# Optimization experiments

Measured on AMD Instinct MI355X. Metric: run time of the kernel, lower is better.

The kernel has to match this reference:

```python
import jax, jax.numpy as jnp
import numpy as np

N, H, C, G = 50000, 16, 8, 128   # nodes, heads, per-head channels, graphs
F_IN, NUM_CLASSES = 128, 2
E = 800000
HC = H * C
NEG_SLOPE = 0.2
BN_EPS = 1e-5


def setup_inputs() -> dict:
    key = jax.random.key(0)
    ks = jax.random.split(key, 32)
    s = 0.1
    p = lambda k, shape: (jax.random.normal(k, shape, jnp.float32) * s)
    inp = {
        "x": jax.random.normal(ks[0], (N, F_IN), jnp.float32),
        "edge_index": jax.random.randint(ks[1], (2, E), 0, N, dtype=jnp.int32),
        "batch": jnp.sort(jax.random.randint(ks[2], (N,), 0, G, dtype=jnp.int32)),
        # GAT layer 1 (in=F_IN)
        "W1": p(ks[3], (F_IN, HC)), "b1": p(ks[4], (HC,)),
        "asrc1": p(ks[5], (H, C)), "adst1": p(ks[6], (H, C)),
        "g1": 1.0 + p(ks[7], (HC,)), "beta1": p(ks[8], (HC,)),
        # GAT layer 2 (in=HC)
        "W2": p(ks[9], (HC, HC)), "b2": p(ks[10], (HC,)),
        "asrc2": p(ks[11], (H, C)), "adst2": p(ks[12], (H, C)),
        "g2": 1.0 + p(ks[13], (HC,)), "beta2": p(ks[14], (HC,)),
        # GAT layer 3
        "W3": p(ks[15], (HC, HC)), "b3": p(ks[16], (HC,)),
        "asrc3": p(ks[17], (H, C)), "adst3": p(ks[18], (H, C)),
        "g3": 1.0 + p(ks[19], (HC,)), "beta3": p(ks[20], (HC,)),
        # final linear + bn4
        "Wl": p(ks[21], (2 * HC, NUM_CLASSES)), "bl": p(ks[22], (NUM_CLASSES,)),
        "g4": 1.0 + p(ks[23], (NUM_CLASSES,)), "beta4": p(ks[24], (NUM_CLASSES,)),
    }
    return inp


def _gat(x, src, dst, W, b, asrc, adst):
    # x: [N, F_in] -> h: [N, H, C]
    h = (x @ W).reshape(N, H, C)
    a_s = jnp.einsum("nhc,hc->nh", h, asrc)  # [N,H]
    a_d = jnp.einsum("nhc,hc->nh", h, adst)
    e = jax.nn.leaky_relu(a_s[src] + a_d[dst], NEG_SLOPE)  # [E',H]
    # per-destination softmax (every node has a self loop -> segments non-empty)
    e_max = jax.ops.segment_max(e, dst, num_segments=N)
    ex = jnp.exp(e - e_max[dst])
    denom = jax.ops.segment_sum(ex, dst, num_segments=N)
    alpha = ex / (denom[dst] + 1e-16)  # [E',H]
    out = jax.ops.segment_sum(h[src] * alpha[:, :, None], dst, num_segments=N)
    return out.reshape(N, HC) + b


def _bn(x, g, beta):
    mu = jnp.mean(x, axis=0)
    var = jnp.mean((x - mu) ** 2, axis=0)  # biased, training-mode BN
    return (x - mu) * jax.lax.rsqrt(var + BN_EPS) * g + beta


def reference(x, edge_index, batch,
              W1, b1, asrc1, adst1, g1, beta1,
              W2, b2, asrc2, adst2, g2, beta2,
              W3, b3, asrc3, adst3, g3, beta3,
              Wl, bl, g4, beta4):
    # add self loops once (add_self_loops=True in every GATConv)
    loop = jnp.arange(N, dtype=edge_index.dtype)
    src = jnp.concatenate([edge_index[0], loop])
    dst = jnp.concatenate([edge_index[1], loop])

    h = jax.nn.relu(_bn(_gat(x, src, dst, W1, b1, asrc1, adst1), g1, beta1))
    h = jax.nn.relu(_bn(_gat(h, src, dst, W2, b2, asrc2, adst2), g2, beta2))
    h = jax.nn.relu(_bn(_gat(h, src, dst, W3, b3, asrc3, adst3), g3, beta3))

    pooled_sum = jax.ops.segment_sum(h, batch, num_segments=G)        # [G,HC]
    cnt = jax.ops.segment_sum(jnp.ones((N,), h.dtype), batch, num_segments=G)
    pooled_mean = pooled_sum / jnp.maximum(cnt, 1.0)[:, None]
    z = jnp.concatenate([pooled_mean, pooled_sum], axis=1)            # [G,2*HC]
    z = z @ Wl + bl
    return _bn(z, g4, beta4)
```

## Files before the change

kernel.cpp:

```cpp
#include <hip/hip_runtime.h>

#define NN 50000
#define NHEADS 16
#define NGRAPH 128
#define NEDGE 800000
#define NEP (NEDGE + NN)

#define EPB 2048
#define NBLK 416
#define NBUK 391

typedef float4 f4;
typedef __attribute__((ext_vector_type(4))) float f32x4;
typedef __attribute__((ext_vector_type(8))) short s8;

__device__ inline unsigned short f2b(float f) {
  union { float f; unsigned u; } v; v.f = f;
  unsigned r = v.u + 0x7FFFu + ((v.u >> 16) & 1u);
  return (unsigned short)(r >> 16);
}
__device__ inline float b2f(unsigned u16) {
  union { unsigned u; float f; } v; v.u = u16 << 16;
  return v.f;
}


__global__ __launch_bounds__(256) void k_hist(const int* __restrict__ ei, int* __restrict__ counts) {
  int i = blockIdx.x * 256 + threadIdx.x;
  if (i >= NEP) return;
  int d = (i < NEDGE) ? ei[NEDGE + i] : (i - NEDGE);
  atomicAdd(&counts[d], 1);
}

__global__ __launch_bounds__(256) void k_scan1(const int* __restrict__ counts, int* __restrict__ row_off, int* __restrict__ blk_tot) {
  __shared__ int buf[256];
  int t = threadIdx.x;
  int i = blockIdx.x * 256 + t;
  int v = (i < NN) ? counts[i] : 0;
  buf[t] = v;
  __syncthreads();
  for (int off = 1; off < 256; off <<= 1) {
    int y = (t >= off) ? buf[t - off] : 0;
    __syncthreads();
    buf[t] += y;
    __syncthreads();
  }
  if (i < NN) row_off[i] = buf[t] - v;
  if (t == 255) blk_tot[blockIdx.x] = buf[255];
}

__global__ __launch_bounds__(256) void k_scan2(const int* __restrict__ blk_tot, int* __restrict__ blk_off, int* __restrict__ row_off, int nb) {
  __shared__ int buf[256];
  int t = threadIdx.x;
  int v = (t < nb) ? blk_tot[t] : 0;
  buf[t] = v;
  __syncthreads();
  for (int off = 1; off < 256; off <<= 1) {
    int y = (t >= off) ? buf[t - off] : 0;
    __syncthreads();
    buf[t] += y;
    __syncthreads();
  }
  if (t < nb) blk_off[t] = buf[t] - v;
  if (t == 255) row_off[NN] = buf[255];
}

__global__ __launch_bounds__(256) void k_scan3(int* __restrict__ row_off, const int* __restrict__ blk_off) {
  int i = blockIdx.x * 256 + threadIdx.x;
  if (i < NN) row_off[i] += blk_off[blockIdx.x];
}


__global__ __launch_bounds__(256) void k_bhist(const int* __restrict__ ei, int* __restrict__ cntmat) {
  __shared__ int hist[NBUK];
  int t = threadIdx.x, b = blockIdx.x;
  for (int k = t; k < NBUK; k += 256) hist[k] = 0;
  __syncthreads();
  int i0 = b * EPB;
  int i1 = i0 + EPB < NEP ? i0 + EPB : NEP;
  for (int i = i0 + t; i < i1; i += 256) {
    int d = (i < NEDGE) ? ei[NEDGE + i] : (i - NEDGE);
    atomicAdd(&hist[d >> 7], 1);
  }
  __syncthreads();
  for (int k = t; k < NBUK; k += 256) cntmat[b * NBUK + k] = hist[k];
}

__global__ __launch_bounds__(512) void k_bscan(int* __restrict__ cntmat) {
  __shared__ int buf[512];
  int t = threadIdx.x, k = blockIdx.x;
  int v = (t < NBLK) ? cntmat[t * NBUK + k] : 0;
  buf[t] = v;
  __syncthreads();
  for (int off = 1; off < 512; off <<= 1) {
    int y = (t >= off) ? buf[t - off] : 0;
    __syncthreads();
    buf[t] += y;
    __syncthreads();
  }
  if (t < NBLK) cntmat[t * NBUK + k] = buf[t] - v;
}

__global__ __launch_bounds__(256) void k_bscatter(const int* __restrict__ ei, const int* __restrict__ cntmat,
                                                  const int* __restrict__ row_off, unsigned* __restrict__ pairs) {
  __shared__ int cur[NBUK];
  int t = threadIdx.x, b = blockIdx.x;
  for (int k = t; k < NBUK; k += 256) cur[k] = row_off[k << 7] + cntmat[b * NBUK + k];
  __syncthreads();
  int i0 = b * EPB;
  int i1 = i0 + EPB < NEP ? i0 + EPB : NEP;
  for (int i = i0 + t; i < i1; i += 256) {
    int s, d;
    if (i < NEDGE) { s = ei[i]; d = ei[NEDGE + i]; }
    else { s = d = i - NEDGE; }
    int pos = atomicAdd(&cur[d >> 7], 1);
    pairs[pos] = ((unsigned)(d & 127) << 16) | (unsigned)s;
  }
}

__global__ __launch_bounds__(256) void k_bfinal(const unsigned* __restrict__ pairs,
                                                const int* __restrict__ row_off, int* __restrict__ colp) {
  __shared__ int cur[128];
  int t = threadIdx.x, k = blockIdx.x;
  int n0 = k << 7;
  if (t < 128 && n0 + t < NN) cur[t] = row_off[n0 + t];
  __syncthreads();
  int nend = (k + 1) << 7; if (nend > NN) nend = NN;
  int p0 = row_off[n0], p1 = row_off[nend];
  for (int i = p0 + t; i < p1; i += 256) {
    unsigned r = pairs[i];
    int pos = atomicAdd(&cur[r >> 16], 1);
    colp[pos] = (int)(r & 0xffffu);
  }
}


__global__ __launch_bounds__(256) void k_cast(const float* __restrict__ X, unsigned short* __restrict__ Xb, int total8) {
  int i = blockIdx.x * 256 + threadIdx.x;
  if (i >= total8) return;
  const f4* X4 = (const f4*)X;
  f4 a = X4[2 * i], b = X4[2 * i + 1];
  uint4 o;
  o.x = (unsigned)f2b(a.x) | ((unsigned)f2b(a.y) << 16);
  o.y = (unsigned)f2b(a.z) | ((unsigned)f2b(a.w) << 16);
  o.z = (unsigned)f2b(b.x) | ((unsigned)f2b(b.y) << 16);
  o.w = (unsigned)f2b(b.z) | ((unsigned)f2b(b.w) << 16);
  ((uint4*)Xb)[i] = o;
}


__global__ __launch_bounds__(256) void k_wt(const float* __restrict__ W0, const float* __restrict__ W1, const float* __restrict__ W2,
                                            unsigned short* __restrict__ T0, unsigned short* __restrict__ T1, unsigned short* __restrict__ T2) {
  int idx = blockIdx.x * 256 + threadIdx.x;
  int L = idx >> 14, r = idx & 16383;
  int n = r >> 7, k = r & 127;
  const float* W = (L == 0) ? W0 : (L == 1) ? W1 : W2;
  unsigned short* T = (L == 0) ? T0 : (L == 1) ? T1 : T2;
  T[n * 128 + k] = f2b(W[k * 128 + n]);
}


__global__ __launch_bounds__(256) void k_gemm(const unsigned short* __restrict__ Xb, const unsigned short* __restrict__ Wt,
                                              unsigned short* __restrict__ Hb) {
  int w = threadIdx.x >> 6, l = threadIdx.x & 63;
  int r0 = blockIdx.x * 128 + w * 32;
  int lr = l & 15, lg = l >> 4;
  f32x4 acc[2][8];
#pragma unroll
  for (int m = 0; m < 2; ++m)
#pragma unroll
    for (int n = 0; n < 8; ++n) acc[m][n] = (f32x4){0.f, 0.f, 0.f, 0.f};

#pragma unroll
  for (int ks = 0; ks < 4; ++ks) {
    int koff = ks * 32 + lg * 8;
    s8 a[2];
#pragma unroll
    for (int m = 0; m < 2; ++m) {
      int row = r0 + m * 16 + lr;
      row = (row < NN) ? row : (NN - 1);
      a[m] = *(const s8*)(Xb + (size_t)row * 128 + koff);
    }
    s8 b[8];
#pragma unroll
    for (int n = 0; n < 8; ++n)
      b[n] = *(const s8*)(Wt + (size_t)(n * 16 + lr) * 128 + koff);
#pragma unroll
    for (int m = 0; m < 2; ++m)
#pragma unroll
      for (int n = 0; n < 8; ++n)
        acc[m][n] = __builtin_amdgcn_mfma_f32_16x16x32_bf16(a[m], b[n], acc[m][n], 0, 0, 0);
  }

#pragma unroll
  for (int m = 0; m < 2; ++m) {
    int rowb = r0 + m * 16 + lg * 4;
#pragma unroll
    for (int n = 0; n < 8; ++n) {
      int colb = n * 16 + lr;
#pragma unroll
      for (int reg = 0; reg < 4; ++reg) {
        int row = rowb + reg;
        if (row < NN) Hb[(size_t)row * 128 + colb] = f2b(acc[m][n][reg]);
      }
    }
  }
}


__global__ __launch_bounds__(256) void k_coef(const unsigned short* __restrict__ Hb, const float* __restrict__ asrc,
                                              const float* __restrict__ adst, unsigned short* __restrict__ Asb, float* __restrict__ Ad) {
  int idx = blockIdx.x * 256 + threadIdx.x;
  if (idx >= NN * NHEADS) return;
  int n = idx >> 4, hd = idx & 15;
  uint4 hv = *(const uint4*)(Hb + (size_t)n * 128 + hd * 8);
  float h0 = b2f(hv.x & 0xffff), h1 = b2f(hv.x >> 16);
  float h2 = b2f(hv.y & 0xffff), h3 = b2f(hv.y >> 16);
  float h4 = b2f(hv.z & 0xffff), h5 = b2f(hv.z >> 16);
  float h6 = b2f(hv.w & 0xffff), h7 = b2f(hv.w >> 16);
  const f4* s4 = (const f4*)(asrc + hd * 8);
  const f4* d4 = (const f4*)(adst + hd * 8);
  f4 sa = s4[0], sb = s4[1], da = d4[0], db = d4[1];
  float as_v = h0 * sa.x + h1 * sa.y + h2 * sa.z + h3 * sa.w + h4 * sb.x + h5 * sb.y + h6 * sb.z + h7 * sb.w;
  float ad_v = h0 * da.x + h1 * da.y + h2 * da.z + h3 * da.w + h4 * db.x + h5 * db.y + h6 * db.z + h7 * db.w;
  Asb[idx] = f2b(as_v);
  Ad[idx] = ad_v;
}


__global__ __launch_bounds__(256) void k_agg(const unsigned short* __restrict__ Hb, const unsigned short* __restrict__ Asb,
                                             const float* __restrict__ Ad,
                                             const int* __restrict__ row_off, const int* __restrict__ col,
                                             unsigned short* __restrict__ Vb) {
  int node = blockIdx.x * 8 + (threadIdx.x >> 5);
  int l = threadIdx.x & 31;
  int h = l & 15, par = l >> 4;
  int e0 = row_off[node], e1 = row_off[node + 1];
  float adh = Ad[node * 16 + h];
  float den = 0.f;
  float acc[8] = {0.f, 0.f, 0.f, 0.f, 0.f, 0.f, 0.f, 0.f};
  int j = e0 + par;
  for (; j + 6 < e1; j += 8) {
    int s0 = col[j], s1 = col[j + 2], s2 = col[j + 4], s3 = col[j + 6];
    float a0 = b2f(Asb[s0 * 16 + h]), a1 = b2f(Asb[s1 * 16 + h]);
    float a2 = b2f(Asb[s2 * 16 + h]), a3 = b2f(Asb[s3 * 16 + h]);
    uint4 p0 = *(const uint4*)(Hb + (size_t)s0 * 128 + h * 8);
    uint4 p1 = *(const uint4*)(Hb + (size_t)s1 * 128 + h * 8);
    uint4 p2 = *(const uint4*)(Hb + (size_t)s2 * 128 + h * 8);
    uint4 p3 = *(const uint4*)(Hb + (size_t)s3 * 128 + h * 8);
    a0 += adh; a1 += adh; a2 += adh; a3 += adh;
    a0 = (a0 > 0.f) ? a0 : 0.2f * a0;  a1 = (a1 > 0.f) ? a1 : 0.2f * a1;
    a2 = (a2 > 0.f) ? a2 : 0.2f * a2;  a3 = (a3 > 0.f) ? a3 : 0.2f * a3;
    float x0 = __expf(a0), x1 = __expf(a1), x2 = __expf(a2), x3 = __expf(a3);
    den += (x0 + x1) + (x2 + x3);
    acc[0] += x0 * b2f(p0.x & 0xffff) + x1 * b2f(p1.x & 0xffff) + x2 * b2f(p2.x & 0xffff) + x3 * b2f(p3.x & 0xffff);
    acc[1] += x0 * b2f(p0.x >> 16)    + x1 * b2f(p1.x >> 16)    + x2 * b2f(p2.x >> 16)    + x3 * b2f(p3.x >> 16);
    acc[2] += x0 * b2f(p0.y & 0xffff) + x1 * b2f(p1.y & 0xffff) + x2 * b2f(p2.y & 0xffff) + x3 * b2f(p3.y & 0xffff);
    acc[3] += x0 * b2f(p0.y >> 16)    + x1 * b2f(p1.y >> 16)    + x2 * b2f(p2.y >> 16)    + x3 * b2f(p3.y >> 16);
    acc[4] += x0 * b2f(p0.z & 0xffff) + x1 * b2f(p1.z & 0xffff) + x2 * b2f(p2.z & 0xffff) + x3 * b2f(p3.z & 0xffff);
    acc[5] += x0 * b2f(p0.z >> 16)    + x1 * b2f(p1.z >> 16)    + x2 * b2f(p2.z >> 16)    + x3 * b2f(p3.z >> 16);
    acc[6] += x0 * b2f(p0.w & 0xffff) + x1 * b2f(p1.w & 0xffff) + x2 * b2f(p2.w & 0xffff) + x3 * b2f(p3.w & 0xffff);
    acc[7] += x0 * b2f(p0.w >> 16)    + x1 * b2f(p1.w >> 16)    + x2 * b2f(p2.w >> 16)    + x3 * b2f(p3.w >> 16);
  }
  for (; j < e1; j += 2) {
    int s0 = col[j];
    float a0 = b2f(Asb[s0 * 16 + h]) + adh;
    uint4 p0 = *(const uint4*)(Hb + (size_t)s0 * 128 + h * 8);
    a0 = (a0 > 0.f) ? a0 : 0.2f * a0;
    float x0 = __expf(a0);
    den += x0;
    acc[0] += x0 * b2f(p0.x & 0xffff);
    acc[1] += x0 * b2f(p0.x >> 16);
    acc[2] += x0 * b2f(p0.y & 0xffff);
    acc[3] += x0 * b2f(p0.y >> 16);
    acc[4] += x0 * b2f(p0.z & 0xffff);
    acc[5] += x0 * b2f(p0.z >> 16);
    acc[6] += x0 * b2f(p0.w & 0xffff);
    acc[7] += x0 * b2f(p0.w >> 16);
  }
  den += __shfl_xor(den, 16);
#pragma unroll
  for (int k = 0; k < 8; ++k) acc[k] += __shfl_xor(acc[k], 16);
  if (par == 0) {
    float inv = 1.f / (den + 1e-16f);
    uint4 o;
    o.x = (unsigned)f2b(acc[0] * inv) | ((unsigned)f2b(acc[1] * inv) << 16);
    o.y = (unsigned)f2b(acc[2] * inv) | ((unsigned)f2b(acc[3] * inv) << 16);
    o.z = (unsigned)f2b(acc[4] * inv) | ((unsigned)f2b(acc[5] * inv) << 16);
    o.w = (unsigned)f2b(acc[6] * inv) | ((unsigned)f2b(acc[7] * inv) << 16);
    *(uint4*)(Vb + (size_t)node * 128 + h * 8) = o;
  }
}


#define BN_CHUNK 391

__global__ __launch_bounds__(256) void k_bnreduce(const unsigned short* __restrict__ Vb, float* __restrict__ partS, float* __restrict__ partQ) {
  int t = threadIdx.x;
  int c4 = t & 31, rs = t >> 5;
  int r0 = blockIdx.x * BN_CHUNK + rs;
  int rend = blockIdx.x * BN_CHUNK + BN_CHUNK;
  if (rend > NN) rend = NN;
  float s0 = 0.f, s1 = 0.f, s2 = 0.f, s3 = 0.f;
  float q0 = 0.f, q1 = 0.f, q2 = 0.f, q3 = 0.f;
  for (int r = r0; r < rend; r += 8) {
    uint2 p = *(const uint2*)(Vb + (size_t)r * 128 + c4 * 4);
    float v0 = b2f(p.x & 0xffff), v1 = b2f(p.x >> 16);
    float v2 = b2f(p.y & 0xffff), v3 = b2f(p.y >> 16);
    s0 += v0; s1 += v1; s2 += v2; s3 += v3;
    q0 += v0 * v0; q1 += v1 * v1; q2 += v2 * v2; q3 += v3 * v3;
  }
  __shared__ float sm[8][32][8];
  sm[rs][c4][0] = s0; sm[rs][c4][1] = s1; sm[rs][c4][2] = s2; sm[rs][c4][3] = s3;
  sm[rs][c4][4] = q0; sm[rs][c4][5] = q1; sm[rs][c4][6] = q2; sm[rs][c4][7] = q3;
  __syncthreads();
  if (t < 32) {
#pragma unroll
    for (int k = 0; k < 4; ++k) {
      float S = 0.f, Q = 0.f;
#pragma unroll
      for (int r = 0; r < 8; ++r) { S += sm[r][t][k]; Q += sm[r][t][4 + k]; }
      partS[blockIdx.x * 128 + t * 4 + k] = S;
      partQ[blockIdx.x * 128 + t * 4 + k] = Q;
    }
  }
}

__global__ __launch_bounds__(512) void k_bnfin(const float* __restrict__ partS, const float* __restrict__ partQ,
                                               const float* __restrict__ gam, const float* __restrict__ bet,
                                               float* __restrict__ sc) {
  int t = threadIdx.x;
  int c = t & 127, q = (t >> 7) & 1, hf = t >> 8;
  const float* src = q ? partQ : partS;
  float s = 0.f;
#pragma unroll 8
  for (int i = hf * 64; i < hf * 64 + 64; ++i) s += src[i * 128 + c];
  __shared__ float sm[512];
  sm[t] = s;
  __syncthreads();
  if (t < 128) {
    float S = sm[t] + sm[t + 256];
    float Q = sm[t + 128] + sm[t + 384];
    float mean = S * (1.f / NN);
    float var = fmaxf(Q * (1.f / NN) - mean * mean, 0.f);
    float sg = gam[t] * rsqrtf(var + 1e-5f);
    sc[t] = sg;
    sc[128 + t] = bet[t] - mean * sg;
  }
}

__global__ __launch_bounds__(256) void k_bnapply(const unsigned short* __restrict__ Vb, unsigned short* __restrict__ Xb,
                                                 const float* __restrict__ sc) {
  int idx = blockIdx.x * 256 + threadIdx.x;
  int c4 = idx & 31;
  uint2 p = ((const uint2*)Vb)[idx];
  f4 s = ((const f4*)sc)[c4], sh = ((const f4*)sc)[32 + c4];
  float v0 = fmaxf(b2f(p.x & 0xffff) * s.x + sh.x, 0.f);
  float v1 = fmaxf(b2f(p.x >> 16)    * s.y + sh.y, 0.f);
  float v2 = fmaxf(b2f(p.y & 0xffff) * s.z + sh.z, 0.f);
  float v3 = fmaxf(b2f(p.y >> 16)    * s.w + sh.w, 0.f);
  uint2 o;
  o.x = (unsigned)f2b(v0) | ((unsigned)f2b(v1) << 16);
  o.y = (unsigned)f2b(v2) | ((unsigned)f2b(v3) << 16);
  ((uint2*)Xb)[idx] = o;
}


__global__ __launch_bounds__(256) void k_gb(const int* __restrict__ batch, int* __restrict__ gstart) {
  int g = threadIdx.x;
  if (g > NGRAPH) return;
  int lo = 0, hi = NN;
  while (lo < hi) { int mid = (lo + hi) >> 1; if (batch[mid] < g) lo = mid + 1; else hi = mid; }
  gstart[g] = lo;
}

__global__ __launch_bounds__(256) void k_pool(const unsigned short* __restrict__ Vb, const int* __restrict__ gstart,
                                              float* __restrict__ pooled) {
  int g = blockIdx.x >> 2, chunk = blockIdx.x & 3;
  int t = threadIdx.x;
  int c4 = t & 31, rs = t >> 5;
  int r0 = gstart[g], r1 = gstart[g + 1];
  float s0 = 0.f, s1 = 0.f, s2 = 0.f, s3 = 0.f;
  for (int r = r0 + chunk + 4 * rs + (c4 & 0) ; r < r1; r += 32) {
    uint2 p = *(const uint2*)(Vb + (size_t)r * 128 + c4 * 4);
    s0 += b2f(p.x & 0xffff); s1 += b2f(p.x >> 16);
    s2 += b2f(p.y & 0xffff); s3 += b2f(p.y >> 16);
  }
  __shared__ float sm[8][32][4];
  sm[rs][c4][0] = s0; sm[rs][c4][1] = s1; sm[rs][c4][2] = s2; sm[rs][c4][3] = s3;
  __syncthreads();
  if (t < 32) {
#pragma unroll
    for (int k = 0; k < 4; ++k) {
      float S = 0.f;
#pragma unroll
      for (int r = 0; r < 8; ++r) S += sm[r][t][k];
      atomicAdd(&pooled[g * 128 + t * 4 + k], S);
    }
  }
}

__global__ __launch_bounds__(256) void k_final(const float* __restrict__ pooled, const int* __restrict__ gstart,
                                               const float* __restrict__ Wl, const float* __restrict__ bl,
                                               const float* __restrict__ g4, const float* __restrict__ b4,
                                               float* __restrict__ out) {
  int t = threadIdx.x;
  int g = t >> 1, cls = t & 1;
  float cnt = fmaxf((float)(gstart[g + 1] - gstart[g]), 1.f);
  float inv = 1.f / cnt;
  float z = bl[cls];
  for (int f = 0; f < 128; ++f) {
    float ps = pooled[g * 128 + f];
    z += ps * inv * Wl[f * 2 + cls] + ps * Wl[(128 + f) * 2 + cls];
  }
  __shared__ float zs[256];
  __shared__ float st[4];
  zs[t] = z;
  __syncthreads();
  if (t < 2) {
    float s = 0.f, s2 = 0.f;
    for (int gg = 0; gg < 128; ++gg) { float v = zs[gg * 2 + t]; s += v; s2 += v * v; }
    float mean = s * (1.f / 128.f);
    float var = s2 * (1.f / 128.f) - mean * mean;
    var = fmaxf(var, 0.f);
    float sc = g4[t] * rsqrtf(var + 1e-5f);
    st[t] = sc; st[2 + t] = b4[t] - mean * sc;
  }
  __syncthreads();
  out[t] = zs[t] * st[cls] + st[2 + cls];
}


extern "C" void kernel_launch(void* const* d_in, const int* in_sizes, int n_in,
                              void* d_out, int out_size, void* d_ws, size_t ws_size,
                              hipStream_t stream) {
  const float* x     = (const float*)d_in[0];
  const int*   ei    = (const int*)d_in[1];
  const int*   batch = (const int*)d_in[2];
  const float* W[3]    = {(const float*)d_in[3],  (const float*)d_in[9],  (const float*)d_in[15]};
  const float* asrc[3] = {(const float*)d_in[5],  (const float*)d_in[11], (const float*)d_in[17]};
  const float* adst[3] = {(const float*)d_in[6],  (const float*)d_in[12], (const float*)d_in[18]};
  const float* gam[3]  = {(const float*)d_in[7],  (const float*)d_in[13], (const float*)d_in[19]};
  const float* bet[3]  = {(const float*)d_in[8],  (const float*)d_in[14], (const float*)d_in[20]};
  const float* Wl    = (const float*)d_in[21];
  const float* bl    = (const float*)d_in[22];
  const float* g4    = (const float*)d_in[23];
  const float* beta4 = (const float*)d_in[24];

  char* ws = (char*)d_ws;
  size_t off = 0;
  auto alloc = [&](size_t bytes) -> void* {
    void* p = (void*)(ws + off);
    off += (bytes + 255) & ~(size_t)255;
    return p;
  };

  int* counts   = (int*)alloc((size_t)NN * 4);
  int* row_off  = (int*)alloc((size_t)(NN + 1) * 4);
  int* col      = (int*)alloc((size_t)NEP * 4);
  int* blk_tot  = (int*)alloc(256 * 4);
  int* blk_off  = (int*)alloc(256 * 4);
  int* cntmat   = (int*)alloc((size_t)NBLK * NBUK * 4);
  unsigned* pairs = (unsigned*)alloc((size_t)NEP * 4);
  unsigned short* Xb = (unsigned short*)alloc((size_t)NN * 128 * 2);
  unsigned short* Hb = (unsigned short*)alloc((size_t)NN * 128 * 2);
  unsigned short* Vb = (unsigned short*)alloc((size_t)NN * 128 * 2);
  unsigned short* Asb = (unsigned short*)alloc((size_t)NN * 16 * 2);
  float* Ad     = (float*)alloc((size_t)NN * 16 * 4);
  unsigned short* Wt0 = (unsigned short*)alloc(16384 * 2);
  unsigned short* Wt1 = (unsigned short*)alloc(16384 * 2);
  unsigned short* Wt2 = (unsigned short*)alloc(16384 * 2);
  const unsigned short* Wt[3] = {Wt0, Wt1, Wt2};
  float* partS  = (float*)alloc(128 * 128 * 4);
  float* partQ  = (float*)alloc(128 * 128 * 4);
  float* bn_sc  = (float*)alloc(256 * 4);
  float* pooled = (float*)alloc((size_t)NGRAPH * 128 * 4);
  int* gstart   = (int*)alloc((size_t)(NGRAPH + 1) * 4);

  hipMemsetAsync(counts, 0, (size_t)NN * 4, stream);
  k_hist<<<(NEP + 255) / 256, 256, 0, stream>>>(ei, counts);
  k_scan1<<<(NN + 255) / 256, 256, 0, stream>>>(counts, row_off, blk_tot);
  k_scan2<<<1, 256, 0, stream>>>(blk_tot, blk_off, row_off, (NN + 255) / 256);
  k_scan3<<<(NN + 255) / 256, 256, 0, stream>>>(row_off, blk_off);

  k_bhist<<<NBLK, 256, 0, stream>>>(ei, cntmat);
  k_bscan<<<NBUK, 512, 0, stream>>>(cntmat);
  k_bscatter<<<NBLK, 256, 0, stream>>>(ei, cntmat, row_off, pairs);
  k_bfinal<<<NBUK, 256, 0, stream>>>(pairs, row_off, col);

  k_wt<<<192, 256, 0, stream>>>(W[0], W[1], W[2], Wt0, Wt1, Wt2);
  k_cast<<<(NN * 16 + 255) / 256, 256, 0, stream>>>(x, Xb, NN * 16);
  k_gb<<<1, 256, 0, stream>>>(batch, gstart);

  hipMemsetAsync(pooled, 0, (size_t)NGRAPH * 128 * 4, stream);

  for (int L = 0; L < 3; ++L) {
    k_gemm<<<(NN + 127) / 128, 256, 0, stream>>>(Xb, Wt[L], Hb);
    k_coef<<<(NN * 16) / 256, 256, 0, stream>>>(Hb, asrc[L], adst[L], Asb, Ad);
    k_agg<<<NN / 8, 256, 0, stream>>>(Hb, Asb, Ad, row_off, col, Vb);
    k_bnreduce<<<128, 256, 0, stream>>>(Vb, partS, partQ);
    k_bnfin<<<1, 512, 0, stream>>>(partS, partQ, gam[L], bet[L], bn_sc);
    k_bnapply<<<(NN * 32) / 256, 256, 0, stream>>>(Vb, Xb, bn_sc);
  }

  k_pool<<<NGRAPH * 4, 256, 0, stream>>>(Xb, gstart, pooled);
  k_final<<<1, 256, 0, stream>>>(pooled, gstart, Wl, bl, g4, beta4, (float*)d_out);
}
```

Baseline: 349.4 us.

## Build CSR from bucket sort alone, merge prep kernels, unroll aggregation deeper

Removes the separate per-node histogram and three-pass scan. Bucket totals are now scanned in k_bbase, and k_bfinal derives per-node row offsets by counting and scanning inside each 128-node bucket. The cast, weight-transpose and graph-boundary kernels are merged into one launch to cut launch overhead. The aggregation edge loop is also unrolled to 8 edges per iteration, giving more loads in flight at the cost of extra registers.

```diff
diff --git a/kernel.cpp b/kernel.cpp
--- a/kernel.cpp
+++ b/kernel.cpp
@@ -9,6 +9,8 @@
 #define EPB 2048
 #define NBLK 416
 #define NBUK 391
+#define CASTB 3125
+#define WTB 192
 
 typedef float4 f4;
 typedef __attribute__((ext_vector_type(4))) float f32x4;
@@ -22,52 +24,6 @@
 __device__ inline float b2f(unsigned u16) {
   union { unsigned u; float f; } v; v.u = u16 << 16;
   return v.f;
-}
-
-
-__global__ __launch_bounds__(256) void k_hist(const int* __restrict__ ei, int* __restrict__ counts) {
-  int i = blockIdx.x * 256 + threadIdx.x;
-  if (i >= NEP) return;
-  int d = (i < NEDGE) ? ei[NEDGE + i] : (i - NEDGE);
-  atomicAdd(&counts[d], 1);
-}
-
-__global__ __launch_bounds__(256) void k_scan1(const int* __restrict__ counts, int* __restrict__ row_off, int* __restrict__ blk_tot) {
-  __shared__ int buf[256];
-  int t = threadIdx.x;
-  int i = blockIdx.x * 256 + t;
-  int v = (i < NN) ? counts[i] : 0;
-  buf[t] = v;
-  __syncthreads();
-  for (int off = 1; off < 256; off <<= 1) {
-    int y = (t >= off) ? buf[t - off] : 0;
-    __syncthreads();
-    buf[t] += y;
-    __syncthreads();
-  }
-  if (i < NN) row_off[i] = buf[t] - v;
-  if (t == 255) blk_tot[blockIdx.x] = buf[255];
-}
-
-__global__ __launch_bounds__(256) void k_scan2(const int* __restrict__ blk_tot, int* __restrict__ blk_off, int* __restrict__ row_off, int nb) {
-  __shared__ int buf[256];
-  int t = threadIdx.x;
-  int v = (t < nb) ? blk_tot[t] : 0;
-  buf[t] = v;
-  __syncthreads();
-  for (int off = 1; off < 256; off <<= 1) {
-    int y = (t >= off) ? buf[t - off] : 0;
-    __syncthreads();
-    buf[t] += y;
-    __syncthreads();
-  }
-  if (t < nb) blk_off[t] = buf[t] - v;
-  if (t == 255) row_off[NN] = buf[255];
-}
-
-__global__ __launch_bounds__(256) void k_scan3(int* __restrict__ row_off, const int* __restrict__ blk_off) {
-  int i = blockIdx.x * 256 + threadIdx.x;
-  if (i < NN) row_off[i] += blk_off[blockIdx.x];
 }
 
 
@@ -86,7 +42,7 @@
   for (int k = t; k < NBUK; k += 256) cntmat[b * NBUK + k] = hist[k];
 }
 
-__global__ __launch_bounds__(512) void k_bscan(int* __restrict__ cntmat) {
+__global__ __launch_bounds__(512) void k_bscan(int* __restrict__ cntmat, int* __restrict__ btotal) {
   __shared__ int buf[512];
   int t = threadIdx.x, k = blockIdx.x;
   int v = (t < NBLK) ? cntmat[t * NBUK + k] : 0;
@@ -99,13 +55,30 @@
     __syncthreads();
   }
   if (t < NBLK) cntmat[t * NBUK + k] = buf[t] - v;
+  if (t == 511) btotal[k] = buf[511];
+}
+
+__global__ __launch_bounds__(512) void k_bbase(const int* __restrict__ btotal, int* __restrict__ bbase) {
+  __shared__ int buf[512];
+  int t = threadIdx.x;
+  int v = (t < NBUK) ? btotal[t] : 0;
+  buf[t] = v;
+  __syncthreads();
+  for (int off = 1; off < 512; off <<= 1) {
+    int y = (t >= off) ? buf[t - off] : 0;
+    __syncthreads();
+    buf[t] += y;
+    __syncthreads();
+  }
+  if (t < NBUK) bbase[t] = buf[t] - v;
+  if (t == 511) bbase[NBUK] = buf[511];
 }
 
 __global__ __launch_bounds__(256) void k_bscatter(const int* __restrict__ ei, const int* __restrict__ cntmat,
-                                                  const int* __restrict__ row_off, unsigned* __restrict__ pairs) {
+                                                  const int* __restrict__ bbase, unsigned* __restrict__ pairs) {
   __shared__ int cur[NBUK];
   int t = threadIdx.x, b = blockIdx.x;
-  for (int k = t; k < NBUK; k += 256) cur[k] = row_off[k << 7] + cntmat[b * NBUK + k];
+  for (int k = t; k < NBUK; k += 256) cur[k] = bbase[k] + cntmat[b * NBUK + k];
   __syncthreads();
   int i0 = b * EPB;
   int i1 = i0 + EPB < NEP ? i0 + EPB : NEP;
@@ -118,15 +91,33 @@
   }
 }
 
-__global__ __launch_bounds__(256) void k_bfinal(const unsigned* __restrict__ pairs,
-                                                const int* __restrict__ row_off, int* __restrict__ colp) {
+__global__ __launch_bounds__(256) void k_bfinal(const unsigned* __restrict__ pairs, const int* __restrict__ bbase,
+                                                int* __restrict__ row_off, int* __restrict__ colp) {
+  __shared__ int cnt[128];
+  __shared__ int buf[128];
   __shared__ int cur[128];
   int t = threadIdx.x, k = blockIdx.x;
   int n0 = k << 7;
-  if (t < 128 && n0 + t < NN) cur[t] = row_off[n0 + t];
-  __syncthreads();
-  int nend = (k + 1) << 7; if (nend > NN) nend = NN;
-  int p0 = row_off[n0], p1 = row_off[nend];
+  if (t < 128) cnt[t] = 0;
+  __syncthreads();
+  int p0 = bbase[k], p1 = bbase[k + 1];
+  for (int i = p0 + t; i < p1; i += 256) atomicAdd(&cnt[pairs[i] >> 16], 1);
+  __syncthreads();
+  if (t < 128) buf[t] = cnt[t];
+  __syncthreads();
+  for (int off = 1; off < 128; off <<= 1) {
+    int y = (t < 128 && t >= off) ? buf[t - off] : 0;
+    __syncthreads();
+    if (t < 128) buf[t] += y;
+    __syncthreads();
+  }
+  if (t < 128) {
+    int excl = buf[t] - cnt[t];
+    cur[t] = p0 + excl;
+    if (n0 + t < NN) row_off[n0 + t] = p0 + excl;
+  }
+  if (k == NBUK - 1 && t == 0) row_off[NN] = p1;
+  __syncthreads();
   for (int i = p0 + t; i < p1; i += 256) {
     unsigned r = pairs[i];
     int pos = atomicAdd(&cur[r >> 16], 1);
@@ -135,28 +126,35 @@
 }
 
 
-__global__ __launch_bounds__(256) void k_cast(const float* __restrict__ X, unsigned short* __restrict__ Xb, int total8) {
-  int i = blockIdx.x * 256 + threadIdx.x;
-  if (i >= total8) return;
-  const f4* X4 = (const f4*)X;
-  f4 a = X4[2 * i], b = X4[2 * i + 1];
-  uint4 o;
-  o.x = (unsigned)f2b(a.x) | ((unsigned)f2b(a.y) << 16);
-  o.y = (unsigned)f2b(a.z) | ((unsigned)f2b(a.w) << 16);
-  o.z = (unsigned)f2b(b.x) | ((unsigned)f2b(b.y) << 16);
-  o.w = (unsigned)f2b(b.z) | ((unsigned)f2b(b.w) << 16);
-  ((uint4*)Xb)[i] = o;
-}
-
-
-__global__ __launch_bounds__(256) void k_wt(const float* __restrict__ W0, const float* __restrict__ W1, const float* __restrict__ W2,
-                                            unsigned short* __restrict__ T0, unsigned short* __restrict__ T1, unsigned short* __restrict__ T2) {
-  int idx = blockIdx.x * 256 + threadIdx.x;
-  int L = idx >> 14, r = idx & 16383;
-  int n = r >> 7, k = r & 127;
-  const float* W = (L == 0) ? W0 : (L == 1) ? W1 : W2;
-  unsigned short* T = (L == 0) ? T0 : (L == 1) ? T1 : T2;
-  T[n * 128 + k] = f2b(W[k * 128 + n]);
+__global__ __launch_bounds__(256) void k_prep(const float* __restrict__ X, unsigned short* __restrict__ Xb,
+                                              const float* __restrict__ W0, const float* __restrict__ W1, const float* __restrict__ W2,
+                                              unsigned short* __restrict__ T0, unsigned short* __restrict__ T1, unsigned short* __restrict__ T2,
+                                              const int* __restrict__ batch, int* __restrict__ gstart) {
+  int b = blockIdx.x, t = threadIdx.x;
+  if (b < CASTB) {
+    int i = b * 256 + t;
+    const f4* X4 = (const f4*)X;
+    f4 a = X4[2 * i], c = X4[2 * i + 1];
+    uint4 o;
+    o.x = (unsigned)f2b(a.x) | ((unsigned)f2b(a.y) << 16);
+    o.y = (unsigned)f2b(a.z) | ((unsigned)f2b(a.w) << 16);
+    o.z = (unsigned)f2b(c.x) | ((unsigned)f2b(c.y) << 16);
+    o.w = (unsigned)f2b(c.z) | ((unsigned)f2b(c.w) << 16);
+    ((uint4*)Xb)[i] = o;
+  } else if (b < CASTB + WTB) {
+    int idx = (b - CASTB) * 256 + t;
+    int L = idx >> 14, r = idx & 16383;
+    int n = r >> 7, kk = r & 127;
+    const float* W = (L == 0) ? W0 : (L == 1) ? W1 : W2;
+    unsigned short* T = (L == 0) ? T0 : (L == 1) ? T1 : T2;
+    T[n * 128 + kk] = f2b(W[kk * 128 + n]);
+  } else {
+    int g = t;
+    if (g > NGRAPH) return;
+    int lo = 0, hi = NN;
+    while (lo < hi) { int mid = (lo + hi) >> 1; if (batch[mid] < g) lo = mid + 1; else hi = mid; }
+    gstart[g] = lo;
+  }
 }
 
 
@@ -240,27 +238,55 @@
   float den = 0.f;
   float acc[8] = {0.f, 0.f, 0.f, 0.f, 0.f, 0.f, 0.f, 0.f};
   int j = e0 + par;
+  for (; j + 14 < e1; j += 16) {
+    int s[8];
+#pragma unroll
+    for (int q = 0; q < 8; ++q) s[q] = col[j + 2 * q];
+    float a[8];
+#pragma unroll
+    for (int q = 0; q < 8; ++q) a[q] = b2f(Asb[s[q] * 16 + h]);
+    uint4 p[8];
+#pragma unroll
+    for (int q = 0; q < 8; ++q) p[q] = *(const uint4*)(Hb + (size_t)s[q] * 128 + h * 8);
+#pragma unroll
+    for (int q = 0; q < 8; ++q) {
+      float e = a[q] + adh;
+      e = (e > 0.f) ? e : 0.2f * e;
+      a[q] = __expf(e);
+      den += a[q];
+    }
+#pragma unroll
+    for (int q = 0; q < 8; ++q) {
+      acc[0] += a[q] * b2f(p[q].x & 0xffff); acc[1] += a[q] * b2f(p[q].x >> 16);
+      acc[2] += a[q] * b2f(p[q].y & 0xffff); acc[3] += a[q] * b2f(p[q].y >> 16);
+      acc[4] += a[q] * b2f(p[q].z & 0xffff); acc[5] += a[q] * b2f(p[q].z >> 16);
+      acc[6] += a[q] * b2f(p[q].w & 0xffff); acc[7] += a[q] * b2f(p[q].w >> 16);
+    }
+  }
   for (; j + 6 < e1; j += 8) {
-    int s0 = col[j], s1 = col[j + 2], s2 = col[j + 4], s3 = col[j + 6];
-    float a0 = b2f(Asb[s0 * 16 + h]), a1 = b2f(Asb[s1 * 16 + h]);
-    float a2 = b2f(Asb[s2 * 16 + h]), a3 = b2f(Asb[s3 * 16 + h]);
-    uint4 p0 = *(const uint4*)(Hb + (size_t)s0 * 128 + h * 8);
-    uint4 p1 = *(const uint4*)(Hb + (size_t)s1 * 128 + h * 8);
-    uint4 p2 = *(const uint4*)(Hb + (size_t)s2 * 128 + h * 8);
-    uint4 p3 = *(const uint4*)(Hb + (size_t)s3 * 128 + h * 8);
-    a0 += adh; a1 += adh; a2 += adh; a3 += adh;
-    a0 = (a0 > 0.f) ? a0 : 0.2f * a0;  a1 = (a1 > 0.f) ? a1 : 0.2f * a1;
-    a2 = (a2 > 0.f) ? a2 : 0.2f * a2;  a3 = (a3 > 0.f) ? a3 : 0.2f * a3;
-    float x0 = __expf(a0), x1 = __expf(a1), x2 = __expf(a2), x3 = __expf(a3);
-    den += (x0 + x1) + (x2 + x3);
-    acc[0] += x0 * b2f(p0.x & 0xffff) + x1 * b2f(p1.x & 0xffff) + x2 * b2f(p2.x & 0xffff) + x3 * b2f(p3.x & 0xffff);
-    acc[1] += x0 * b2f(p0.x >> 16)    + x1 * b2f(p1.x >> 16)    + x2 * b2f(p2.x >> 16)    + x3 * b2f(p3.x >> 16);
-    acc[2] += x0 * b2f(p0.y & 0xffff) + x1 * b2f(p1.y & 0xffff) + x2 * b2f(p2.y & 0xffff) + x3 * b2f(p3.y & 0xffff);
-    acc[3] += x0 * b2f(p0.y >> 16)    + x1 * b2f(p1.y >> 16)    + x2 * b2f(p2.y >> 16)    + x3 * b2f(p3.y >> 16);
-    acc[4] += x0 * b2f(p0.z & 0xffff) + x1 * b2f(p1.z & 0xffff) + x2 * b2f(p2.z & 0xffff) + x3 * b2f(p3.z & 0xffff);
-    acc[5] += x0 * b2f(p0.z >> 16)    + x1 * b2f(p1.z >> 16)    + x2 * b2f(p2.z >> 16)    + x3 * b2f(p3.z >> 16);
-    acc[6] += x0 * b2f(p0.w & 0xffff) + x1 * b2f(p1.w & 0xffff) + x2 * b2f(p2.w & 0xffff) + x3 * b2f(p3.w & 0xffff);
-    acc[7] += x0 * b2f(p0.w >> 16)    + x1 * b2f(p1.w >> 16)    + x2 * b2f(p2.w >> 16)    + x3 * b2f(p3.w >> 16);
+    int s[4];
+#pragma unroll
+    for (int q = 0; q < 4; ++q) s[q] = col[j + 2 * q];
+    float a[4];
+#pragma unroll
+    for (int q = 0; q < 4; ++q) a[q] = b2f(Asb[s[q] * 16 + h]);
+    uint4 p[4];
+#pragma unroll
+    for (int q = 0; q < 4; ++q) p[q] = *(const uint4*)(Hb + (size_t)s[q] * 128 + h * 8);
+#pragma unroll
+    for (int q = 0; q < 4; ++q) {
+      float e = a[q] + adh;
+      e = (e > 0.f) ? e : 0.2f * e;
+      a[q] = __expf(e);
+      den += a[q];
+    }
+#pragma unroll
+    for (int q = 0; q < 4; ++q) {
+      acc[0] += a[q] * b2f(p[q].x & 0xffff); acc[1] += a[q] * b2f(p[q].x >> 16);
+      acc[2] += a[q] * b2f(p[q].y & 0xffff); acc[3] += a[q] * b2f(p[q].y >> 16);
+      acc[4] += a[q] * b2f(p[q].z & 0xffff); acc[5] += a[q] * b2f(p[q].z >> 16);
+      acc[6] += a[q] * b2f(p[q].w & 0xffff); acc[7] += a[q] * b2f(p[q].w >> 16);
+    }
   }
   for (; j < e1; j += 2) {
     int s0 = col[j];
@@ -366,14 +392,6 @@
 }
 
 
-__global__ __launch_bounds__(256) void k_gb(const int* __restrict__ batch, int* __restrict__ gstart) {
-  int g = threadIdx.x;
-  if (g > NGRAPH) return;
-  int lo = 0, hi = NN;
-  while (lo < hi) { int mid = (lo + hi) >> 1; if (batch[mid] < g) lo = mid + 1; else hi = mid; }
-  gstart[g] = lo;
-}
-
 __global__ __launch_bounds__(256) void k_pool(const unsigned short* __restrict__ Vb, const int* __restrict__ gstart,
                                               float* __restrict__ pooled) {
   int g = blockIdx.x >> 2, chunk = blockIdx.x & 3;
@@ -381,7 +399,7 @@
   int c4 = t & 31, rs = t >> 5;
   int r0 = gstart[g], r1 = gstart[g + 1];
   float s0 = 0.f, s1 = 0.f, s2 = 0.f, s3 = 0.f;
-  for (int r = r0 + chunk + 4 * rs + (c4 & 0) ; r < r1; r += 32) {
+  for (int r = r0 + chunk + 4 * rs; r < r1; r += 32) {
     uint2 p = *(const uint2*)(Vb + (size_t)r * 128 + c4 * 4);
     s0 += b2f(p.x & 0xffff); s1 += b2f(p.x >> 16);
     s2 += b2f(p.y & 0xffff); s3 += b2f(p.y >> 16);
@@ -455,12 +473,11 @@
     return p;
   };
 
-  int* counts   = (int*)alloc((size_t)NN * 4);
   int* row_off  = (int*)alloc((size_t)(NN + 1) * 4);
   int* col      = (int*)alloc((size_t)NEP * 4);
-  int* blk_tot  = (int*)alloc(256 * 4);
-  int* blk_off  = (int*)alloc(256 * 4);
   int* cntmat   = (int*)alloc((size_t)NBLK * NBUK * 4);
+  int* btotal   = (int*)alloc((size_t)NBUK * 4);
+  int* bbase    = (int*)alloc((size_t)(NBUK + 1) * 4);
   unsigned* pairs = (unsigned*)alloc((size_t)NEP * 4);
   unsigned short* Xb = (unsigned short*)alloc((size_t)NN * 128 * 2);
   unsigned short* Hb = (unsigned short*)alloc((size_t)NN * 128 * 2);
@@ -477,20 +494,13 @@
   float* pooled = (float*)alloc((size_t)NGRAPH * 128 * 4);
   int* gstart   = (int*)alloc((size_t)(NGRAPH + 1) * 4);
 
-  hipMemsetAsync(counts, 0, (size_t)NN * 4, stream);
-  k_hist<<<(NEP + 255) / 256, 256, 0, stream>>>(ei, counts);
-  k_scan1<<<(NN + 255) / 256, 256, 0, stream>>>(counts, row_off, blk_tot);
-  k_scan2<<<1, 256, 0, stream>>>(blk_tot, blk_off, row_off, (NN + 255) / 256);
-  k_scan3<<<(NN + 255) / 256, 256, 0, stream>>>(row_off, blk_off);
-
   k_bhist<<<NBLK, 256, 0, stream>>>(ei, cntmat);
-  k_bscan<<<NBUK, 512, 0, stream>>>(cntmat);
-  k_bscatter<<<NBLK, 256, 0, stream>>>(ei, cntmat, row_off, pairs);
-  k_bfinal<<<NBUK, 256, 0, stream>>>(pairs, row_off, col);
-
-  k_wt<<<192, 256, 0, stream>>>(W[0], W[1], W[2], Wt0, Wt1, Wt2);
-  k_cast<<<(NN * 16 + 255) / 256, 256, 0, stream>>>(x, Xb, NN * 16);
-  k_gb<<<1, 256, 0, stream>>>(batch, gstart);
+  k_bscan<<<NBUK, 512, 0, stream>>>(cntmat, btotal);
+  k_bbase<<<1, 512, 0, stream>>>(btotal, bbase);
+  k_bscatter<<<NBLK, 256, 0, stream>>>(ei, cntmat, bbase, pairs);
+  k_bfinal<<<NBUK, 256, 0, stream>>>(pairs, bbase, row_off, col);
+
+  k_prep<<<CASTB + WTB + 1, 256, 0, stream>>>(x, Xb, W[0], W[1], W[2], Wt0, Wt1, Wt2, batch, gstart);
 
   hipMemsetAsync(pooled, 0, (size_t)NGRAPH * 128 * 4, stream);
 
```

Measured after the change: 311.1 us. -11.0%, faster.
